# Optimization experiments

Hardware: AMD Instinct MI355X
Metric: run time of the kernel (lower is better)

The kernel has to match this reference:

```python
import jax, jax.numpy as jnp
import numpy as np

N_NODES = 50000
N_EDGES = 1600000
IN_F = 256
OUT_F = 128
N_REL = 500
NEG_SLOPE = 0.2
EPS = 1e-10


def setup_inputs() -> dict:
    key = jax.random.key(0)
    ks = jax.random.split(key, 7)
    h = jax.random.normal(ks[0], (N_NODES, IN_F), dtype=jnp.float32)
    rows = jax.random.randint(ks[1], (N_EDGES,), 0, N_NODES)
    cols = jax.random.randint(ks[2], (N_EDGES,), 0, N_NODES)
    edge_types = jax.random.randint(ks[3], (N_EDGES,), 0, N_REL)
    # learned params (xavier-ish small scale)
    W = jax.random.normal(ks[4], (IN_F, OUT_F), dtype=jnp.float32) * 0.05
    rel_emb = jax.random.normal(ks[5], (N_REL, OUT_F), dtype=jnp.float32) * 0.05
    a = jax.random.normal(ks[6], (2 * OUT_F + OUT_F,), dtype=jnp.float32) * 0.05
    return {"h": h, "rows": rows, "cols": cols, "edge_types": edge_types,
            "W": W, "rel_emb": rel_emb, "a": a}


def reference(h, rows, cols, edge_types, W, rel_emb, a):
    N = h.shape[0]
    d = W.shape[1]
    Wh = h @ W                                   # [N, out]
    # a^T [Wh_i || Wh_j || r] decomposed to avoid materializing the concat
    a_i, a_j, a_r = a[:d], a[d:2 * d], a[2 * d:]
    s_node_i = Wh @ a_i                          # [N]
    s_node_j = Wh @ a_j                          # [N]
    s_rel = rel_emb @ a_r                        # [R]
    e = s_node_i[rows] + s_node_j[cols] + s_rel[edge_types]   # [E]
    e = jax.nn.leaky_relu(e, negative_slope=NEG_SLOPE)
    e = e - jnp.max(e)                           # global max-shift as in original
    exp_e = jnp.exp(e)
    sum_exp = jax.ops.segment_sum(exp_e, rows, num_segments=N)  # [N]
    alpha = exp_e / (sum_exp[rows] + EPS)        # [E]  (dropout is identity in eval)
    # sparse matmul: h'_i = sum_{j in N(i)} alpha_ij * Wh_j
    h_prime = jax.ops.segment_sum(alpha[:, None] * Wh[cols], rows, num_segments=N)
    return jax.nn.elu(h_prime)
```

## Files before the change

kernel.cpp:

```cpp
#include <hip/hip_runtime.h>

#define N_NODES 50000
#define N_EDGES 1600000
#define IN_F    256
#define OUT_F   128
#define N_REL   500
#define NEG_SLOPE 0.2f
#define EPS_F   1e-10f
#define GEMM_ROWS 64

#define NB       1563
#define CAP      1408
#define BIN_CHUNK 4096
#define NBIN_BLK 391

typedef __attribute__((ext_vector_type(8))) __bf16 bf16x8;
typedef __attribute__((ext_vector_type(4))) float f32x4;

static __device__ __forceinline__ float bf2f(unsigned short u) {
    unsigned v = ((unsigned)u) << 16;
    float f;
    __builtin_memcpy(&f, &v, 4);
    return f;
}
static __device__ __forceinline__ unsigned short f2bf(float f) {
    unsigned u;
    __builtin_memcpy(&u, &f, 4);
    unsigned rounding = 0x7fffu + ((u >> 16) & 1u);
    u += rounding;
    return (unsigned short)(u >> 16);
}

__global__ __launch_bounds__(256) void wconv_k(
    const float* __restrict__ W,
    const float* __restrict__ a,
    unsigned short* __restrict__ WbfT,
    unsigned short* __restrict__ wai_bf, unsigned short* __restrict__ waj_bf)
{
    int wid  = threadIdx.x >> 6;
    int lane = threadIdx.x & 63;
    int k    = blockIdx.x * 4 + wid;
    int n0   = lane * 2;
    float2 wv2 = *(const float2*)(W + (size_t)k * OUT_F + n0);
    WbfT[(size_t)n0 * IN_F + k]       = f2bf(wv2.x);
    WbfT[(size_t)(n0 + 1) * IN_F + k] = f2bf(wv2.y);
    float si = wv2.x * a[n0] + wv2.y * a[n0 + 1];
    float sj = wv2.x * a[OUT_F + n0] + wv2.y * a[OUT_F + n0 + 1];
    #pragma unroll
    for (int off = 32; off; off >>= 1) {
        si += __shfl_xor(si, off, 64);
        sj += __shfl_xor(sj, off, 64);
    }
    if (lane == 0) { wai_bf[k] = f2bf(si); waj_bf[k] = f2bf(sj); }
}

__global__ __launch_bounds__(256) void srel_k(
    const float* __restrict__ rel_emb,
    const float* __restrict__ a,
    float* __restrict__ s_rel)
{
    int rid  = blockIdx.x * 4 + (threadIdx.x >> 6);
    int lane = threadIdx.x & 63;
    if (rid >= N_REL) return;
    float2 re = *(const float2*)(rel_emb + (size_t)rid * OUT_F + 2 * lane);
    float2 ar = *(const float2*)(a + 2 * OUT_F + 2 * lane);
    float sr = re.x * ar.x + re.y * ar.y;
    #pragma unroll
    for (int off = 32; off; off >>= 1) sr += __shfl_xor(sr, off, 64);
    if (lane == 0) s_rel[rid] = sr;
}

__global__ __launch_bounds__(256) void gemm_wh(
    const float* __restrict__ h,
    const unsigned short* __restrict__ WbfT,
    const unsigned short* __restrict__ wai_bf, const unsigned short* __restrict__ waj_bf,
    unsigned short* __restrict__ Whb,
    float* __restrict__ s_i, float* __restrict__ s_j)
{
    __shared__ unsigned short Ash[GEMM_ROWS * IN_F];
    const int t    = threadIdx.x;
    const int wv   = t >> 6;
    const int lane = t & 63;
    const int quad = lane >> 4;
    const int l15  = lane & 15;
    const int r0   = blockIdx.x * GEMM_ROWS;

    bf16x8 Bfrag[2][8];
    #pragma unroll
    for (int ct2 = 0; ct2 < 2; ++ct2) {
        int n = 32 * wv + 16 * ct2 + l15;
        #pragma unroll
        for (int ks = 0; ks < 8; ++ks)
            Bfrag[ct2][ks] = *(const bf16x8*)(WbfT + (size_t)n * IN_F + 32 * ks + 8 * quad);
    }
    bf16x8 Sfrag[8];
    if (wv == 0) {
        const unsigned short* ssrc = (l15 == 0) ? wai_bf : waj_bf;
        #pragma unroll
        for (int ks = 0; ks < 8; ++ks) {
            if (l15 < 2) Sfrag[ks] = *(const bf16x8*)(ssrc + 32 * ks + 8 * quad);
            else         Sfrag[ks] = (bf16x8)(__bf16)0.0f;
        }
    }

    #pragma unroll
    for (int i = 0; i < 16; ++i) {
        int q   = t + 256 * i;
        int row = q >> 6;
        int k   = (q & 63) * 4;
        int gr  = r0 + row;
        float4 v = make_float4(0.f, 0.f, 0.f, 0.f);
        if (gr < N_NODES) v = *(const float4*)(h + (size_t)gr * IN_F + k);
        int ks = k >> 5, qd = (k >> 3) & 3, j = k & 7;
        int rg = row >> 4, m15 = row & 15;
        int off = ((((rg << 3) + ks) << 6) + ((qd << 4) | m15)) * 8 + j;
        ushort4 p;
        p.x = f2bf(v.x); p.y = f2bf(v.y); p.z = f2bf(v.z); p.w = f2bf(v.w);
        *(ushort4*)(Ash + off) = p;
    }
    __syncthreads();

    #pragma unroll 1
    for (int rg = 0; rg < 4; ++rg) {
        const unsigned short* base = Ash + (((rg << 3) << 6) + lane) * 8;
        bf16x8 Afrag[8];
        #pragma unroll
        for (int ks = 0; ks < 8; ++ks)
            Afrag[ks] = *(const bf16x8*)(base + (ks << 6) * 8);
        f32x4 acc0 = {0.f, 0.f, 0.f, 0.f};
        f32x4 acc1 = {0.f, 0.f, 0.f, 0.f};
        #pragma unroll
        for (int ks = 0; ks < 8; ++ks) {
            acc0 = __builtin_amdgcn_mfma_f32_16x16x32_bf16(Afrag[ks], Bfrag[0][ks], acc0, 0, 0, 0);
            acc1 = __builtin_amdgcn_mfma_f32_16x16x32_bf16(Afrag[ks], Bfrag[1][ks], acc1, 0, 0, 0);
        }
        #pragma unroll
        for (int reg = 0; reg < 4; ++reg) {
            int gr = r0 + 16 * rg + quad * 4 + reg;
            if (gr < N_NODES) {
                Whb[(size_t)gr * OUT_F + 32 * wv + l15]      = f2bf(acc0[reg]);
                Whb[(size_t)gr * OUT_F + 32 * wv + 16 + l15] = f2bf(acc1[reg]);
            }
        }
        if (wv == 0) {
            f32x4 acc2 = {0.f, 0.f, 0.f, 0.f};
            #pragma unroll
            for (int ks = 0; ks < 8; ++ks)
                acc2 = __builtin_amdgcn_mfma_f32_16x16x32_bf16(Afrag[ks], Sfrag[ks], acc2, 0, 0, 0);
            #pragma unroll
            for (int reg = 0; reg < 4; ++reg) {
                int gr = r0 + 16 * rg + quad * 4 + reg;
                if (gr < N_NODES) {
                    if (l15 == 0) s_i[gr] = acc2[reg];
                    else if (l15 == 1) s_j[gr] = acc2[reg];
                }
            }
        }
    }
}

__global__ __launch_bounds__(256) void bin_k(
    const int* __restrict__ rows, const int* __restrict__ cols, const int* __restrict__ types,
    const float* __restrict__ s_i, const float* __restrict__ s_j, const float* __restrict__ s_rel,
    int* __restrict__ cnt, uint2* __restrict__ epk)
{
    __shared__ int hist[NB];
    __shared__ int lbase[NB];
    __shared__ int cur[NB];
    __shared__ float srl[N_REL];
    int t = threadIdx.x;
    for (int i = t; i < NB; i += 256) { hist[i] = 0; cur[i] = 0; }
    for (int i = t; i < N_REL; i += 256) srl[i] = s_rel[i];
    __syncthreads();

    int base = blockIdx.x * BIN_CHUNK;
    float cw[16];
    unsigned cm[16];
    #pragma unroll
    for (int i = 0; i < 16; ++i) {
        int e = base + t + 256 * i;
        if (e < N_EDGES) {
            int r = rows[e], c = cols[e], ty = types[e];
            float v = s_i[r] + s_j[c] + srl[ty];
            v = (v > 0.f) ? v : NEG_SLOPE * v;
            cw[i] = __expf(v);
            int b = r >> 5;
            cm[i] = (unsigned)c | ((unsigned)(r & 31) << 16) | ((unsigned)b << 21);
            atomicAdd(&hist[b], 1);
        } else {
            cw[i] = 0.f;
            cm[i] = 0xffffffffu;
        }
    }
    __syncthreads();
    for (int i = t; i < NB; i += 256)
        if (hist[i] > 0) lbase[i] = atomicAdd(&cnt[i], hist[i]);
    __syncthreads();
    #pragma unroll
    for (int i = 0; i < 16; ++i) {
        int e = base + t + 256 * i;
        if (e < N_EDGES) {
            int b = cm[i] >> 21;
            int loc = lbase[b] + atomicAdd(&cur[b], 1);
            if (loc < CAP)
                epk[(size_t)b * CAP + loc] = make_uint2(__float_as_uint(cw[i]), cm[i] & 0x1fffffu);
        }
    }
}

__global__ __launch_bounds__(256) void bucket_agg(
    const int* __restrict__ cnt, const uint2* __restrict__ epk,
    const unsigned short* __restrict__ Whb,
    float* __restrict__ out)
{
    __shared__ uint2 sorted[CAP];
    __shared__ int hist[32];
    __shared__ int offs[33];
    __shared__ int cur[32];

    const int t    = threadIdx.x;
    const int wid  = t >> 6;
    const int lane = t & 63;
    const int b    = blockIdx.x;
    const int n    = min(cnt[b], CAP);
    const uint2* ep = epk + (size_t)b * CAP;
    const unsigned* Whu = (const unsigned*)Whb;

    if (t < 32) { hist[t] = 0; }
    __syncthreads();

    uint2 rec[6];
    #pragma unroll
    for (int i = 0; i < 6; ++i) {
        int idx = t + 256 * i;
        rec[i] = (idx < n) ? ep[idx] : make_uint2(0u, 0xffffffffu);
    }
    #pragma unroll
    for (int i = 0; i < 6; ++i)
        if (rec[i].y != 0xffffffffu) atomicAdd(&hist[(rec[i].y >> 16) & 31], 1);
    __syncthreads();
    if (wid == 0 && lane < 32) {
        int v = hist[lane];
        #pragma unroll
        for (int off = 1; off < 32; off <<= 1) {
            int u = __shfl_up(v, off, 64);
            if (lane >= off) v += u;
        }
        offs[lane + 1] = v;
        if (lane == 0) offs[0] = 0;
        cur[lane] = v - hist[lane];
    }
    __syncthreads();
    #pragma unroll
    for (int i = 0; i < 6; ++i) {
        if (rec[i].y != 0xffffffffu) {
            int pos = atomicAdd(&cur[(rec[i].y >> 16) & 31], 1);
            sorted[pos] = rec[i];
        }
    }
    __syncthreads();

    #pragma unroll 1
    for (int rl = 0; rl < 8; ++rl) {
        int row = wid * 8 + rl;
        int i = offs[row], e1 = offs[row + 1];
        float s = 0.f, x0 = 0.f, x1 = 0.f;
        for (; i + 8 <= e1; i += 8) {
            uint2 rc[8];
            #pragma unroll
            for (int j = 0; j < 8; ++j) rc[j] = sorted[i + j];
            unsigned p[8];
            #pragma unroll
            for (int j = 0; j < 8; ++j)
                p[j] = Whu[(size_t)(rc[j].y & 0xffffu) * 64 + lane];
            #pragma unroll
            for (int j = 0; j < 8; ++j) {
                float w = __uint_as_float(rc[j].x);
                s  += w;
                x0 += w * bf2f(p[j] & 0xffffu);
                x1 += w * bf2f(p[j] >> 16);
            }
        }
        for (; i + 4 <= e1; i += 4) {
            uint2 r0 = sorted[i], r1 = sorted[i + 1], r2 = sorted[i + 2], r3 = sorted[i + 3];
            unsigned p0 = Whu[(size_t)(r0.y & 0xffffu) * 64 + lane];
            unsigned p1 = Whu[(size_t)(r1.y & 0xffffu) * 64 + lane];
            unsigned p2 = Whu[(size_t)(r2.y & 0xffffu) * 64 + lane];
            unsigned p3 = Whu[(size_t)(r3.y & 0xffffu) * 64 + lane];
            float w0 = __uint_as_float(r0.x), w1 = __uint_as_float(r1.x);
            float w2 = __uint_as_float(r2.x), w3 = __uint_as_float(r3.x);
            s  += (w0 + w1) + (w2 + w3);
            x0 += w0 * bf2f(p0 & 0xffffu) + w1 * bf2f(p1 & 0xffffu)
                + w2 * bf2f(p2 & 0xffffu) + w3 * bf2f(p3 & 0xffffu);
            x1 += w0 * bf2f(p0 >> 16) + w1 * bf2f(p1 >> 16)
                + w2 * bf2f(p2 >> 16) + w3 * bf2f(p3 >> 16);
        }
        for (; i < e1; ++i) {
            uint2 r0 = sorted[i];
            unsigned p0 = Whu[(size_t)(r0.y & 0xffffu) * 64 + lane];
            float w0 = __uint_as_float(r0.x);
            s  += w0;
            x0 += w0 * bf2f(p0 & 0xffffu);
            x1 += w0 * bf2f(p0 >> 16);
        }
        int grow = b * 32 + row;
        if (grow < N_NODES) {
            float inv = 1.f / (s + EPS_F);
            float v0 = x0 * inv, v1 = x1 * inv;
            v0 = (v0 > 0.f) ? v0 : (__expf(v0) - 1.f);
            v1 = (v1 > 0.f) ? v1 : (__expf(v1) - 1.f);
            *(float2*)(out + (size_t)grow * OUT_F + 2 * lane) = make_float2(v0, v1);
        }
    }
}

extern "C" void kernel_launch(void* const* d_in, const int* in_sizes, int n_in,
                              void* d_out, int out_size, void* d_ws, size_t ws_size,
                              hipStream_t stream)
{
    const float* h     = (const float*)d_in[0];
    const int*   rows  = (const int*)d_in[1];
    const int*   cols  = (const int*)d_in[2];
    const int*   types = (const int*)d_in[3];
    const float* W     = (const float*)d_in[4];
    const float* rel   = (const float*)d_in[5];
    const float* a     = (const float*)d_in[6];

    char* ws = (char*)d_ws;
    size_t off = 0;
    auto alloc = [&](size_t bytes) -> void* {
        void* p = ws + off;
        off = (off + bytes + 255) & ~(size_t)255;
        return p;
    };
    unsigned short* Whb   = (unsigned short*)alloc((size_t)N_NODES * OUT_F * 2);
    unsigned short* WbfT  = (unsigned short*)alloc((size_t)IN_F * OUT_F * 2);
    unsigned short* wai_bf = (unsigned short*)alloc((size_t)IN_F * 2);
    unsigned short* waj_bf = (unsigned short*)alloc((size_t)IN_F * 2);
    float* s_i    = (float*)alloc((size_t)N_NODES * 4);
    float* s_j    = (float*)alloc((size_t)N_NODES * 4);
    float* s_rel  = (float*)alloc((size_t)N_REL * 4);
    int*   cnt    = (int*)alloc((size_t)NB * 4);
    uint2* epk    = (uint2*)alloc((size_t)NB * CAP * 8);
    (void)ws_size; (void)in_sizes; (void)n_in; (void)out_size;

    hipMemsetAsync(cnt, 0, (size_t)NB * 4, stream);

    wconv_k<<<64, 256, 0, stream>>>(W, a, WbfT, wai_bf, waj_bf);
    srel_k<<<(N_REL + 3) / 4, 256, 0, stream>>>(rel, a, s_rel);
    gemm_wh<<<(N_NODES + GEMM_ROWS - 1) / GEMM_ROWS, 256, 0, stream>>>(
        h, WbfT, wai_bf, waj_bf, Whb, s_i, s_j);
    bin_k<<<NBIN_BLK, 256, 0, stream>>>(rows, cols, types, s_i, s_j, s_rel, cnt, epk);
    bucket_agg<<<NB, 256, 0, stream>>>(cnt, epk, Whb, (float*)d_out);
}
```

Baseline: 231.6 us.

## Halve bucket size, split wave across two edges, load GEMM A directly

Buckets now cover 16 destination rows instead of 32, which doubles the number of aggregation blocks and halves the per-bucket capacity. In the aggregation kernel each wave splits into two half-waves that process alternate edges, each lane gathering 8 bytes (4 bf16) per edge; the halves are then combined with a cross-half shuffle. The GEMM drops its LDS staging of h and builds bf16 A fragments straight from global loads. The aim is more parallelism and wider gathers in aggregation plus less LDS traffic and sync in the GEMM, at the risk of redundant global loads of h across the four waves, and of overflow if more than 768 edges land in one bucket.

```diff
diff --git a/kernel.cpp b/kernel.cpp
--- a/kernel.cpp
+++ b/kernel.cpp
@@ -9,13 +9,14 @@
 #define EPS_F   1e-10f
 #define GEMM_ROWS 64
 
-#define NB       1563
-#define CAP      1408
+#define NB       3125
+#define CAP      768
 #define BIN_CHUNK 4096
 #define NBIN_BLK 391
 
 typedef __attribute__((ext_vector_type(8))) __bf16 bf16x8;
 typedef __attribute__((ext_vector_type(4))) float f32x4;
+typedef __attribute__((ext_vector_type(2))) float f32x2;
 
 static __device__ __forceinline__ float bf2f(unsigned short u) {
     unsigned v = ((unsigned)u) << 16;
@@ -77,7 +78,6 @@
     unsigned short* __restrict__ Whb,
     float* __restrict__ s_i, float* __restrict__ s_j)
 {
-    __shared__ unsigned short Ash[GEMM_ROWS * IN_F];
     const int t    = threadIdx.x;
     const int wv   = t >> 6;
     const int lane = t & 63;
@@ -103,30 +103,21 @@
         }
     }
 
-    #pragma unroll
-    for (int i = 0; i < 16; ++i) {
-        int q   = t + 256 * i;
-        int row = q >> 6;
-        int k   = (q & 63) * 4;
-        int gr  = r0 + row;
-        float4 v = make_float4(0.f, 0.f, 0.f, 0.f);
-        if (gr < N_NODES) v = *(const float4*)(h + (size_t)gr * IN_F + k);
-        int ks = k >> 5, qd = (k >> 3) & 3, j = k & 7;
-        int rg = row >> 4, m15 = row & 15;
-        int off = ((((rg << 3) + ks) << 6) + ((qd << 4) | m15)) * 8 + j;
-        ushort4 p;
-        p.x = f2bf(v.x); p.y = f2bf(v.y); p.z = f2bf(v.z); p.w = f2bf(v.w);
-        *(ushort4*)(Ash + off) = p;
-    }
-    __syncthreads();
-
     #pragma unroll 1
     for (int rg = 0; rg < 4; ++rg) {
-        const unsigned short* base = Ash + (((rg << 3) << 6) + lane) * 8;
+        int row = r0 + rg * 16 + l15;
+        if (row > N_NODES - 1) row = N_NODES - 1;
+        const float* hp = h + (size_t)row * IN_F + quad * 8;
         bf16x8 Afrag[8];
         #pragma unroll
-        for (int ks = 0; ks < 8; ++ks)
-            Afrag[ks] = *(const bf16x8*)(base + (ks << 6) * 8);
+        for (int ks = 0; ks < 8; ++ks) {
+            float4 u0 = *(const float4*)(hp + ks * 32);
+            float4 u1 = *(const float4*)(hp + ks * 32 + 4);
+            bf16x8 af;
+            af[0] = (__bf16)u0.x; af[1] = (__bf16)u0.y; af[2] = (__bf16)u0.z; af[3] = (__bf16)u0.w;
+            af[4] = (__bf16)u1.x; af[5] = (__bf16)u1.y; af[6] = (__bf16)u1.z; af[7] = (__bf16)u1.w;
+            Afrag[ks] = af;
+        }
         f32x4 acc0 = {0.f, 0.f, 0.f, 0.f};
         f32x4 acc1 = {0.f, 0.f, 0.f, 0.f};
         #pragma unroll
@@ -184,8 +175,8 @@
             float v = s_i[r] + s_j[c] + srl[ty];
             v = (v > 0.f) ? v : NEG_SLOPE * v;
             cw[i] = __expf(v);
-            int b = r >> 5;
-            cm[i] = (unsigned)c | ((unsigned)(r & 31) << 16) | ((unsigned)b << 21);
+            int b = r >> 4;
+            cm[i] = (unsigned)c | ((unsigned)(r & 15) << 16) | ((unsigned)b << 20);
             atomicAdd(&hist[b], 1);
         } else {
             cw[i] = 0.f;
@@ -200,23 +191,23 @@
     for (int i = 0; i < 16; ++i) {
         int e = base + t + 256 * i;
         if (e < N_EDGES) {
-            int b = cm[i] >> 21;
+            int b = cm[i] >> 20;
             int loc = lbase[b] + atomicAdd(&cur[b], 1);
             if (loc < CAP)
-                epk[(size_t)b * CAP + loc] = make_uint2(__float_as_uint(cw[i]), cm[i] & 0x1fffffu);
-        }
-    }
-}
-
-__global__ __launch_bounds__(256) void bucket_agg(
+                epk[(size_t)b * CAP + loc] = make_uint2(__float_as_uint(cw[i]), cm[i] & 0xfffffu);
+        }
+    }
+}
+
+__global__ __launch_bounds__(256, 8) void bucket_agg(
     const int* __restrict__ cnt, const uint2* __restrict__ epk,
     const unsigned short* __restrict__ Whb,
     float* __restrict__ out)
 {
     __shared__ uint2 sorted[CAP];
-    __shared__ int hist[32];
-    __shared__ int offs[33];
-    __shared__ int cur[32];
+    __shared__ int hist[16];
+    __shared__ int offs[17];
+    __shared__ int cur[16];
 
     const int t    = threadIdx.x;
     const int wid  = t >> 6;
@@ -224,25 +215,24 @@
     const int b    = blockIdx.x;
     const int n    = min(cnt[b], CAP);
     const uint2* ep = epk + (size_t)b * CAP;
-    const unsigned* Whu = (const unsigned*)Whb;
-
-    if (t < 32) { hist[t] = 0; }
-    __syncthreads();
-
-    uint2 rec[6];
-    #pragma unroll
-    for (int i = 0; i < 6; ++i) {
+
+    if (t < 16) hist[t] = 0;
+    __syncthreads();
+
+    uint2 rec[3];
+    #pragma unroll
+    for (int i = 0; i < 3; ++i) {
         int idx = t + 256 * i;
         rec[i] = (idx < n) ? ep[idx] : make_uint2(0u, 0xffffffffu);
     }
     #pragma unroll
-    for (int i = 0; i < 6; ++i)
-        if (rec[i].y != 0xffffffffu) atomicAdd(&hist[(rec[i].y >> 16) & 31], 1);
-    __syncthreads();
-    if (wid == 0 && lane < 32) {
+    for (int i = 0; i < 3; ++i)
+        if (rec[i].y != 0xffffffffu) atomicAdd(&hist[(rec[i].y >> 16) & 15], 1);
+    __syncthreads();
+    if (wid == 0 && lane < 16) {
         int v = hist[lane];
         #pragma unroll
-        for (int off = 1; off < 32; off <<= 1) {
+        for (int off = 1; off < 16; off <<= 1) {
             int u = __shfl_up(v, off, 64);
             if (lane >= off) v += u;
         }
@@ -252,64 +242,92 @@
     }
     __syncthreads();
     #pragma unroll
-    for (int i = 0; i < 6; ++i) {
+    for (int i = 0; i < 3; ++i) {
         if (rec[i].y != 0xffffffffu) {
-            int pos = atomicAdd(&cur[(rec[i].y >> 16) & 31], 1);
-            sorted[pos] = rec[i];
-        }
-    }
-    __syncthreads();
+            int pos = atomicAdd(&cur[(rec[i].y >> 16) & 15], 1);
+            sorted[pos] = make_uint2(rec[i].x, (rec[i].y & 0xffffu) << 8);
+        }
+    }
+    __syncthreads();
+
+    const unsigned hh = lane >> 5;
+    const unsigned lb = (unsigned)(lane & 31) << 3;
+    const char* wbase = (const char*)Whb;
 
     #pragma unroll 1
-    for (int rl = 0; rl < 8; ++rl) {
-        int row = wid * 8 + rl;
-        int i = offs[row], e1 = offs[row + 1];
-        float s = 0.f, x0 = 0.f, x1 = 0.f;
-        for (; i + 8 <= e1; i += 8) {
-            uint2 rc[8];
-            #pragma unroll
-            for (int j = 0; j < 8; ++j) rc[j] = sorted[i + j];
-            unsigned p[8];
-            #pragma unroll
-            for (int j = 0; j < 8; ++j)
-                p[j] = Whu[(size_t)(rc[j].y & 0xffffu) * 64 + lane];
-            #pragma unroll
-            for (int j = 0; j < 8; ++j) {
+    for (int rl = 0; rl < 4; ++rl) {
+        const int row = wid * 4 + rl;
+        int i = offs[row];
+        const int e1 = offs[row + 1];
+        f32x2 a01 = {0.f, 0.f};
+        f32x2 a23 = {0.f, 0.f};
+        float s = 0.f;
+
+        for (; i + 12 <= e1; i += 12) {
+            uint2 rc[6];
+            #pragma unroll
+            for (int j = 0; j < 6; ++j) rc[j] = sorted[i + 2 * j + hh];
+            uint2 pk[6];
+            #pragma unroll
+            for (int j = 0; j < 6; ++j)
+                pk[j] = *(const uint2*)(wbase + (rc[j].y + lb));
+            #pragma unroll
+            for (int j = 0; j < 6; ++j) {
                 float w = __uint_as_float(rc[j].x);
-                s  += w;
-                x0 += w * bf2f(p[j] & 0xffffu);
-                x1 += w * bf2f(p[j] >> 16);
+                unsigned p0 = pk[j].x, p1 = pk[j].y;
+                a01.x = __builtin_fmaf(__uint_as_float(p0 << 16),          w, a01.x);
+                a01.y = __builtin_fmaf(__uint_as_float(p0 & 0xffff0000u),  w, a01.y);
+                a23.x = __builtin_fmaf(__uint_as_float(p1 << 16),          w, a23.x);
+                a23.y = __builtin_fmaf(__uint_as_float(p1 & 0xffff0000u),  w, a23.y);
+                s += w;
             }
         }
         for (; i + 4 <= e1; i += 4) {
-            uint2 r0 = sorted[i], r1 = sorted[i + 1], r2 = sorted[i + 2], r3 = sorted[i + 3];
-            unsigned p0 = Whu[(size_t)(r0.y & 0xffffu) * 64 + lane];
-            unsigned p1 = Whu[(size_t)(r1.y & 0xffffu) * 64 + lane];
-            unsigned p2 = Whu[(size_t)(r2.y & 0xffffu) * 64 + lane];
-            unsigned p3 = Whu[(size_t)(r3.y & 0xffffu) * 64 + lane];
-            float w0 = __uint_as_float(r0.x), w1 = __uint_as_float(r1.x);
-            float w2 = __uint_as_float(r2.x), w3 = __uint_as_float(r3.x);
-            s  += (w0 + w1) + (w2 + w3);
-            x0 += w0 * bf2f(p0 & 0xffffu) + w1 * bf2f(p1 & 0xffffu)
-                + w2 * bf2f(p2 & 0xffffu) + w3 * bf2f(p3 & 0xffffu);
-            x1 += w0 * bf2f(p0 >> 16) + w1 * bf2f(p1 >> 16)
-                + w2 * bf2f(p2 >> 16) + w3 * bf2f(p3 >> 16);
-        }
-        for (; i < e1; ++i) {
-            uint2 r0 = sorted[i];
-            unsigned p0 = Whu[(size_t)(r0.y & 0xffffu) * 64 + lane];
-            float w0 = __uint_as_float(r0.x);
-            s  += w0;
-            x0 += w0 * bf2f(p0 & 0xffffu);
-            x1 += w0 * bf2f(p0 >> 16);
-        }
-        int grow = b * 32 + row;
-        if (grow < N_NODES) {
+            uint2 rc0 = sorted[i + hh];
+            uint2 rc1 = sorted[i + 2 + hh];
+            uint2 pk0 = *(const uint2*)(wbase + (rc0.y + lb));
+            uint2 pk1 = *(const uint2*)(wbase + (rc1.y + lb));
+            float w0 = __uint_as_float(rc0.x);
+            float w1 = __uint_as_float(rc1.x);
+            a01.x = __builtin_fmaf(__uint_as_float(pk0.x << 16),         w0, a01.x);
+            a01.y = __builtin_fmaf(__uint_as_float(pk0.x & 0xffff0000u), w0, a01.y);
+            a23.x = __builtin_fmaf(__uint_as_float(pk0.y << 16),         w0, a23.x);
+            a23.y = __builtin_fmaf(__uint_as_float(pk0.y & 0xffff0000u), w0, a23.y);
+            a01.x = __builtin_fmaf(__uint_as_float(pk1.x << 16),         w1, a01.x);
+            a01.y = __builtin_fmaf(__uint_as_float(pk1.x & 0xffff0000u), w1, a01.y);
+            a23.x = __builtin_fmaf(__uint_as_float(pk1.y << 16),         w1, a23.x);
+            a23.y = __builtin_fmaf(__uint_as_float(pk1.y & 0xffff0000u), w1, a23.y);
+            s += w0 + w1;
+        }
+        for (; i < e1; i += 2) {
+            int idx = i + (int)hh;
+            uint2 r0 = (idx < e1) ? sorted[idx] : make_uint2(0u, 0u);
+            uint2 pk0 = *(const uint2*)(wbase + (r0.y + lb));
+            float w = __uint_as_float(r0.x);
+            a01.x = __builtin_fmaf(__uint_as_float(pk0.x << 16),         w, a01.x);
+            a01.y = __builtin_fmaf(__uint_as_float(pk0.x & 0xffff0000u), w, a01.y);
+            a23.x = __builtin_fmaf(__uint_as_float(pk0.y << 16),         w, a23.x);
+            a23.y = __builtin_fmaf(__uint_as_float(pk0.y & 0xffff0000u), w, a23.y);
+            s += w;
+        }
+
+        s     += __shfl_xor(s, 32, 64);
+        a01.x += __shfl_xor(a01.x, 32, 64);
+        a01.y += __shfl_xor(a01.y, 32, 64);
+        a23.x += __shfl_xor(a23.x, 32, 64);
+        a23.y += __shfl_xor(a23.y, 32, 64);
+
+        if (hh == 0) {
+            const int grow = b * 16 + row;
             float inv = 1.f / (s + EPS_F);
-            float v0 = x0 * inv, v1 = x1 * inv;
+            float v0 = a01.x * inv, v1 = a01.y * inv;
+            float v2 = a23.x * inv, v3 = a23.y * inv;
             v0 = (v0 > 0.f) ? v0 : (__expf(v0) - 1.f);
             v1 = (v1 > 0.f) ? v1 : (__expf(v1) - 1.f);
-            *(float2*)(out + (size_t)grow * OUT_F + 2 * lane) = make_float2(v0, v1);
+            v2 = (v2 > 0.f) ? v2 : (__expf(v2) - 1.f);
+            v3 = (v3 > 0.f) ? v3 : (__expf(v3) - 1.f);
+            *(float4*)(out + (size_t)grow * OUT_F + ((lane & 31) << 2)) =
+                make_float4(v0, v1, v2, v3);
         }
     }
 }
```

Result: slower. 239.2 us (+3.3%).
